# Performance work log

Hardware: AMD Instinct MI355X
Metric: run time of the kernel (lower is better)

The kernel has to match this reference:

```python
import jax, jax.numpy as jnp
import numpy as np

HEIGHT = 16   # RoIRotate(height=16)
MAX_W = 128   # static padded width (== max achievable new_width given box generation)


def setup_inputs() -> dict:
    key = jax.random.key(0)
    k1, k2, k3, k4, k5 = jax.random.split(key, 5)
    B, C, H, W, N = 8, 32, 512, 512, 64
    image = jax.random.normal(k1, (B, C, H, W), dtype=jnp.float32)
    # Box geometry: heights in [8,40], aspect ratio in [1,8] -> new_width in [16,128]
    bh = jax.random.uniform(k2, (B, N), minval=8.0, maxval=40.0)
    ar = jax.random.uniform(k3, (B, N), minval=1.0, maxval=8.0)
    bw = bh * ar
    left = jax.random.uniform(k4, (B, N)) * (W - 1.0 - bw)
    top = jax.random.uniform(k5, (B, N)) * (H - 1.0 - bh)
    theta = jnp.zeros((B, N), dtype=jnp.float32)  # theta unused by the module
    boxes = jnp.stack([left, top, left + bw, top + bh, theta], axis=-1).astype(jnp.float32)
    return {"image": image, "boxes": boxes}


def _roi_rotate(image, boxes):
    B, C, H, W = image.shape
    left, top, right, bottom = boxes[..., 0], boxes[..., 1], boxes[..., 2], boxes[..., 3]
    bw = right - left                       # base_widths  [B,N]
    bh = bottom - top                       # base_heights [B,N]
    # aspect = bw/bh; NaN (0/0) -> width 0, as in the torch code
    aspect = jnp.where(bh > 0, bw / jnp.maximum(bh, 1e-6), 0.0)
    new_w = jnp.clip((aspect * HEIGHT).astype(jnp.int32), 0, MAX_W)  # [B,N]
    each_w = bw / jnp.maximum(new_w - 1, 1).astype(jnp.float32)
    each_h = bh / float(HEIGHT - 1)
    kx = jnp.arange(MAX_W, dtype=jnp.float32)
    ky = jnp.arange(HEIGHT, dtype=jnp.float32)
    xx = kx[None, None, :] * each_w[..., None] + left[..., None]   # [B,N,MAX_W]
    yy = ky[None, None, :] * each_h[..., None] + top[..., None]    # [B,N,HEIGHT]
    x0 = jnp.clip(jnp.floor(xx).astype(jnp.int32), 0, W - 1)
    x1 = jnpp_clip = jnp.clip(x0 + 1, 0, W - 1)
    y0 = jnp.clip(jnp.floor(yy).astype(jnp.int32), 0, H - 1)
    y1 = jnp.clip(y0 + 1, 0, H - 1)
    im_flat = image.reshape(B, C, H * W)

    def g(imf, ylin, xlin):
        # imf [C,H*W], ylin [N,Hh], xlin [N,Wm] -> [C,N,Hh,Wm]
        lin = ylin[:, :, None] * W + xlin[:, None, :]
        return imf[:, lin]

    gather = jax.vmap(g)
    Ia = gather(im_flat, y0, x0)  # [B,C,N,Hh,Wm]
    Ib = gather(im_flat, y1, x0)
    Ic = gather(im_flat, y0, x1)
    Id = gather(im_flat, y1, x1)
    # weights use the clamped corner coordinates, matching the torch code
    wx1 = x1.astype(jnp.float32) - xx       # [B,N,MAX_W]
    wx0 = xx - x0.astype(jnp.float32)
    wy1 = y1.astype(jnp.float32) - yy       # [B,N,HEIGHT]
    wy0 = yy - y0.astype(jnp.float32)
    WX1 = wx1[:, None, :, None, :]
    WX0 = wx0[:, None, :, None, :]
    WY1 = wy1[:, None, :, :, None]
    WY0 = wy0[:, None, :, :, None]
    res = Ia * WX1 * WY1 + Ib * WX1 * WY0 + Ic * WX0 * WY1 + Id * WX0 * WY0
    mask = jnp.arange(MAX_W)[None, None, :] < new_w[..., None]    # [B,N,MAX_W]
    res = res * mask[:, None, :, None, :].astype(res.dtype)
    res = jnp.transpose(res, (0, 2, 1, 3, 4))                      # [B,N,C,Hh,Wm]
    return res, mask.astype(jnp.uint8)


def reference(image, boxes):
    return _roi_rotate(image, boxes)
```

## Files before the change

### kernel.cpp

```cpp
#include <hip/hip_runtime.h>

#define BB 8
#define CC 32
#define HH 512
#define WW 512
#define NN 64
#define RH 16
#define RW 128

#define RES_ELEMS ((size_t)BB * NN * CC * RH * RW)

__global__ __launch_bounds__(256) void roi_main(const float* __restrict__ img,
                                                const float* __restrict__ boxes,
                                                float* __restrict__ out) {
    const int tid = threadIdx.x;
    const int k   = tid & (RW - 1);
    const int jlo = tid >> 7;
    const unsigned blk = blockIdx.x;
    const int c = (blk >> 3) & (CC - 1);
    const int j = ((blk & 7) << 1) | jlo;
    const int n = (blk >> 8) & (NN - 1);
    const int b = blk >> 14;

    const float* bx = boxes + ((size_t)(b * NN + n) * 5);
    const float left   = bx[0];
    const float top    = bx[1];
    const float right  = bx[2];
    const float bottom = bx[3];

    const float bw = right - left;
    const float bh = bottom - top;
    const float aspect = (bh > 0.0f) ? (bw / fmaxf(bh, 1e-6f)) : 0.0f;
    int new_w = (int)(aspect * (float)RH);
    new_w = min(max(new_w, 0), RW);
    const float each_w = bw / (float)max(new_w - 1, 1);
    const float each_h = bh / (float)(RH - 1);

    float val = 0.0f;
    if (k < new_w) {
        const float xx = (float)k * each_w + left;
        const float yy = (float)j * each_h + top;

        int x0 = (int)floorf(xx);
        x0 = min(max(x0, 0), WW - 1);
        const int x1 = min(x0 + 1, WW - 1);
        int y0 = (int)floorf(yy);
        y0 = min(max(y0, 0), HH - 1);
        const int y1 = min(y0 + 1, HH - 1);

        const float* imf = img + ((size_t)(b * CC + c) * (HH * WW));
        const float Ia = imf[(size_t)y0 * WW + x0];
        const float Ib = imf[(size_t)y1 * WW + x0];
        const float Ic = imf[(size_t)y0 * WW + x1];
        const float Id = imf[(size_t)y1 * WW + x1];

        const float wx1 = (float)x1 - xx;
        const float wx0 = xx - (float)x0;
        const float wy1 = (float)y1 - yy;
        const float wy0 = yy - (float)y0;

        val = Ia * wx1 * wy1 + Ib * wx1 * wy0 + Ic * wx0 * wy1 + Id * wx0 * wy0;
    }

    out[(size_t)blk * 256 + tid] = val;
}

__global__ __launch_bounds__(256) void roi_mask(const float* __restrict__ boxes,
                                                float* __restrict__ mout) {
    const int t  = blockIdx.x * 256 + threadIdx.x;
    const int k  = t & (RW - 1);
    const int bn = t >> 7;
    const float* bx = boxes + (size_t)bn * 5;
    const float bw = bx[2] - bx[0];
    const float bh = bx[3] - bx[1];
    const float aspect = (bh > 0.0f) ? (bw / fmaxf(bh, 1e-6f)) : 0.0f;
    int new_w = (int)(aspect * (float)RH);
    new_w = min(max(new_w, 0), RW);
    mout[t] = (k < new_w) ? 1.0f : 0.0f;
}

extern "C" void kernel_launch(void* const* d_in, const int* in_sizes, int n_in,
                              void* d_out, int out_size, void* d_ws, size_t ws_size,
                              hipStream_t stream) {
    const float* img   = (const float*)d_in[0];
    const float* boxes = (const float*)d_in[1];
    float* out = (float*)d_out;

    const int main_blocks = (int)(RES_ELEMS / 256);
    roi_main<<<main_blocks, 256, 0, stream>>>(img, boxes, out);

    const int mask_blocks = (BB * NN * RW) / 256;
    roi_mask<<<mask_blocks, 256, 0, stream>>>(boxes, out + RES_ELEMS);
}
```

Baseline: 417.9 us.

## Fuse mask into main kernel and compute eight rows per thread

Merges the mask kernel into the main RoI kernel, removing one launch. Each block now covers a whole (b,n,c) slice and each thread loops over eight output rows, so the box math and x-coordinate work are done once per thread instead of once per row. The gather now loads adjacent pixel pairs from a clamped base and picks the right one with a select at the right edge. This cuts block count and redundant index math, at the cost of less parallelism per block and more serial work per thread.

```diff
diff --git a/kernel.cpp b/kernel.cpp
--- a/kernel.cpp
+++ b/kernel.cpp
@@ -10,73 +10,74 @@
 
 #define RES_ELEMS ((size_t)BB * NN * CC * RH * RW)
 
-__global__ __launch_bounds__(256) void roi_main(const float* __restrict__ img,
-                                                const float* __restrict__ boxes,
-                                                float* __restrict__ out) {
+__global__ __launch_bounds__(256) void roi_fused(const float* __restrict__ img,
+                                                 const float* __restrict__ boxes,
+                                                 float* __restrict__ out,
+                                                 float* __restrict__ mout) {
     const int tid = threadIdx.x;
     const int k   = tid & (RW - 1);
-    const int jlo = tid >> 7;
+    const int jh  = tid >> 7;
     const unsigned blk = blockIdx.x;
-    const int c = (blk >> 3) & (CC - 1);
-    const int j = ((blk & 7) << 1) | jlo;
-    const int n = (blk >> 8) & (NN - 1);
-    const int b = blk >> 14;
+    const int c   = blk & (CC - 1);
+    const int bn  = blk >> 5;
+    const int b   = bn >> 6;
 
-    const float* bx = boxes + ((size_t)(b * NN + n) * 5);
-    const float left   = bx[0];
-    const float top    = bx[1];
-    const float right  = bx[2];
-    const float bottom = bx[3];
-
-    const float bw = right - left;
-    const float bh = bottom - top;
+    const float* bx = boxes + (size_t)bn * 5;
+    const float left = bx[0];
+    const float top  = bx[1];
+    const float bw   = bx[2] - left;
+    const float bh   = bx[3] - top;
     const float aspect = (bh > 0.0f) ? (bw / fmaxf(bh, 1e-6f)) : 0.0f;
     int new_w = (int)(aspect * (float)RH);
     new_w = min(max(new_w, 0), RW);
     const float each_w = bw / (float)max(new_w - 1, 1);
     const float each_h = bh / (float)(RH - 1);
 
-    float val = 0.0f;
+    float* outp = out + (size_t)blk * (RH * RW) + (size_t)jh * (8 * RW) + k;
+
+    if (c == 0 && jh == 0)
+        mout[(size_t)bn * RW + k] = (k < new_w) ? 1.0f : 0.0f;
+
     if (k < new_w) {
         const float xx = (float)k * each_w + left;
-        const float yy = (float)j * each_h + top;
-
         int x0 = (int)floorf(xx);
         x0 = min(max(x0, 0), WW - 1);
-        const int x1 = min(x0 + 1, WW - 1);
-        int y0 = (int)floorf(yy);
-        y0 = min(max(y0, 0), HH - 1);
-        const int y1 = min(y0 + 1, HH - 1);
-
-        const float* imf = img + ((size_t)(b * CC + c) * (HH * WW));
-        const float Ia = imf[(size_t)y0 * WW + x0];
-        const float Ib = imf[(size_t)y1 * WW + x0];
-        const float Ic = imf[(size_t)y0 * WW + x1];
-        const float Id = imf[(size_t)y1 * WW + x1];
-
+        const int x1  = min(x0 + 1, WW - 1);
+        const int xg  = min(x0, WW - 2);
+        const bool edge = (x0 == WW - 1);
         const float wx1 = (float)x1 - xx;
         const float wx0 = xx - (float)x0;
-        const float wy1 = (float)y1 - yy;
-        const float wy0 = yy - (float)y0;
 
-        val = Ia * wx1 * wy1 + Ib * wx1 * wy0 + Ic * wx0 * wy1 + Id * wx0 * wy0;
+        const float* imf = img + ((size_t)(b * CC + c) * (HH * WW)) + xg;
+
+        #pragma unroll
+        for (int jj = 0; jj < 8; ++jj) {
+            const int j = jh * 8 + jj;
+            const float yy = (float)j * each_h + top;
+            int y0 = (int)floorf(yy);
+            y0 = min(max(y0, 0), HH - 1);
+            const int y1 = min(y0 + 1, HH - 1);
+            const float wy1 = (float)y1 - yy;
+            const float wy0 = yy - (float)y0;
+
+            const float* rowA = imf + (size_t)y0 * WW;
+            const float* rowB = imf + (size_t)y1 * WW;
+            const float a0 = rowA[0], a1 = rowA[1];
+            const float b0 = rowB[0], b1 = rowB[1];
+            const float Ia = edge ? a1 : a0;
+            const float Ic = a1;
+            const float Ib = edge ? b1 : b0;
+            const float Id = b1;
+
+            const float val = Ia * wx1 * wy1 + Ib * wx1 * wy0
+                            + Ic * wx0 * wy1 + Id * wx0 * wy0;
+            outp[(size_t)jj * RW] = val;
+        }
+    } else {
+        #pragma unroll
+        for (int jj = 0; jj < 8; ++jj)
+            outp[(size_t)jj * RW] = 0.0f;
     }
-
-    out[(size_t)blk * 256 + tid] = val;
-}
-
-__global__ __launch_bounds__(256) void roi_mask(const float* __restrict__ boxes,
-                                                float* __restrict__ mout) {
-    const int t  = blockIdx.x * 256 + threadIdx.x;
-    const int k  = t & (RW - 1);
-    const int bn = t >> 7;
-    const float* bx = boxes + (size_t)bn * 5;
-    const float bw = bx[2] - bx[0];
-    const float bh = bx[3] - bx[1];
-    const float aspect = (bh > 0.0f) ? (bw / fmaxf(bh, 1e-6f)) : 0.0f;
-    int new_w = (int)(aspect * (float)RH);
-    new_w = min(max(new_w, 0), RW);
-    mout[t] = (k < new_w) ? 1.0f : 0.0f;
 }
 
 extern "C" void kernel_launch(void* const* d_in, const int* in_sizes, int n_in,
@@ -84,11 +85,9 @@
                               hipStream_t stream) {
     const float* img   = (const float*)d_in[0];
     const float* boxes = (const float*)d_in[1];
-    float* out = (float*)d_out;
+    float* out  = (float*)d_out;
+    float* mout = out + RES_ELEMS;
 
-    const int main_blocks = (int)(RES_ELEMS / 256);
-    roi_main<<<main_blocks, 256, 0, stream>>>(img, boxes, out);
-
-    const int mask_blocks = (BB * NN * RW) / 256;
-    roi_mask<<<mask_blocks, 256, 0, stream>>>(boxes, out + RES_ELEMS);
+    const int blocks = BB * NN * CC;
+    roi_fused<<<blocks, 256, 0, stream>>>(img, boxes, out, mout);
 }
```

Measured after the change: 379.4 us. 9.2% less time.
